# Kernel tuning notes

Hardware: AMD Instinct MI355X
Metric: run time of the kernel (lower is better)

Reference implementation:

```python
import jax, jax.numpy as jnp
import numpy as np

E, D, H, T = 8, 1024, 2048, 2048  # num_expert, d_model, d_hidden, tokens

def setup_inputs() -> dict:
    key = jax.random.key(0)
    ks = jax.random.split(key, 7)
    return {
        "moe_inp": jax.random.normal(ks[0], (T, D), jnp.float32),
        "Wg": jax.random.normal(ks[1], (D, E), jnp.float32) * 0.02,
        "bg": jnp.zeros((E,), jnp.float32),
        "W1": jax.random.normal(ks[2], (E, D, H), jnp.float32) * 0.02,
        "b1": jnp.zeros((E, H), jnp.float32),
        "W2": jax.random.normal(ks[3], (E, H, D), jnp.float32) * 0.02,
        "b2": jnp.zeros((E, D), jnp.float32),
        "top_k": 2,
    }

def reference(moe_inp, Wg, bg, W1, b1, W2, b2, top_k):
    # NaiveGate: linear gate, top-k select, softmax over the selected logits
    logits = moe_inp @ Wg + bg                      # [T, E]
    top_vals, top_idx = jax.lax.top_k(logits, top_k)  # [T, k]
    gate_score = jax.nn.softmax(top_vals, axis=-1)    # [T, k]

    # Exact (no capacity drop) MoE: scan over experts, mask-combine.
    # Equivalent math to scatter -> per-expert FFN -> gather -> bmm(gate_score, ...).
    def body(acc, xs):
        e, w1, bb1, w2, bb2 = xs
        h = jax.nn.gelu(moe_inp @ w1 + bb1)          # [T, H]
        y = h @ w2 + bb2                             # [T, D]
        w = jnp.sum(jnp.where(top_idx == e, gate_score, 0.0), axis=-1)  # [T]
        return acc + w[:, None] * y, None

    init = jnp.zeros_like(moe_inp)
    xs = (jnp.arange(E), W1, b1, W2, b2)
    moe_outp, _ = jax.lax.scan(body, init, xs)
    return moe_outp, top_idx
```

## Files before the change

### kernel.cpp

```cpp
#include <hip/hip_runtime.h>
#include <stdint.h>

#define T_TOK 2048
#define D_DIM 1024
#define H_DIM 2048
#define N_EXP 8
#define MAXS  4608

#define WS_CNT    0
#define WS_BTOK   256
#define WS_BW     (WS_BTOK + N_EXP*2048*4)
#define WS_XG     (WS_BW + N_EXP*2048*4)
#define WS_HBUF   (WS_XG + (size_t)MAXS*1024*2)
#define WS_W1T    (WS_HBUF + (size_t)MAXS*2048*2)
#define WS_W2T    (WS_W1T + (size_t)N_EXP*1024*2048*2)

typedef __bf16 bf16x8 __attribute__((ext_vector_type(8)));
typedef float  f32x4  __attribute__((ext_vector_type(4)));

__device__ __forceinline__ unsigned short f2bf(float f) {
  unsigned int u = __float_as_uint(f);
  u += 0x7fffu + ((u >> 16) & 1u);
  return (unsigned short)(u >> 16);
}

__device__ __forceinline__ float gelu_tanh(float x) {
  float u = 0.7978845608028654f * (x + 0.044715f * x * x * x);
  return 0.5f * x * (1.0f + tanhf(u));
}

__global__ void zero_kernel(float4* __restrict__ out4, int* __restrict__ cnt) {
  int i = blockIdx.x * 256 + threadIdx.x;
  out4[i] = make_float4(0.f, 0.f, 0.f, 0.f);
  if (blockIdx.x == 0 && threadIdx.x < N_EXP) cnt[threadIdx.x] = 0;
}

__global__ void gate_kernel(const float* __restrict__ x, const float* __restrict__ Wg,
                            const float* __restrict__ bg, float* __restrict__ out_idx,
                            int* __restrict__ cnt, int* __restrict__ btok,
                            float* __restrict__ bw) {
  const int lane = threadIdx.x & 63;
  const int t = blockIdx.x * 4 + (threadIdx.x >> 6);
  float p[8];
#pragma unroll
  for (int i = 0; i < 8; ++i) p[i] = 0.f;
  const float* xr = x + (size_t)t * D_DIM;
  for (int i = lane; i < D_DIM; i += 64) {
    const float xv = xr[i];
    const float4 wa = ((const float4*)(Wg + i * 8))[0];
    const float4 wb = ((const float4*)(Wg + i * 8))[1];
    p[0] += xv * wa.x; p[1] += xv * wa.y; p[2] += xv * wa.z; p[3] += xv * wa.w;
    p[4] += xv * wb.x; p[5] += xv * wb.y; p[6] += xv * wb.z; p[7] += xv * wb.w;
  }
#pragma unroll
  for (int off = 32; off > 0; off >>= 1) {
#pragma unroll
    for (int i = 0; i < 8; ++i) p[i] += __shfl_xor(p[i], off);
  }
  if (lane == 0) {
#pragma unroll
    for (int i = 0; i < 8; ++i) p[i] += bg[i];
    int i0 = 0; float v0 = p[0];
#pragma unroll
    for (int i = 1; i < 8; ++i) if (p[i] > v0) { v0 = p[i]; i0 = i; }
    int i1 = -1; float v1 = -3.4e38f;
#pragma unroll
    for (int i = 0; i < 8; ++i) if (i != i0 && p[i] > v1) { v1 = p[i]; i1 = i; }
    const float ex = expf(v1 - v0);
    const float inv = 1.f / (1.f + ex);
    out_idx[t * 2 + 0] = (float)i0;
    out_idx[t * 2 + 1] = (float)i1;
    int s0 = atomicAdd(&cnt[i0], 1);
    btok[i0 * 2048 + s0] = t; bw[i0 * 2048 + s0] = inv;
    int s1 = atomicAdd(&cnt[i1], 1);
    btok[i1 * 2048 + s1] = t; bw[i1 * 2048 + s1] = ex * inv;
  }
}

__global__ void transpose_cvt(const float* __restrict__ W1, unsigned short* __restrict__ W1t,
                              const float* __restrict__ W2, unsigned short* __restrict__ W2t) {
  const int set = blockIdx.z;
  const int e = blockIdx.y;
  const int lin = blockIdx.x;
  const int R = set ? H_DIM : D_DIM;
  const int C = set ? D_DIM : H_DIM;
  const int tx = set ? (lin & 15) : (lin & 31);
  const int ty = set ? (lin >> 4) : (lin >> 5);
  const float* in = (set ? W2 : W1) + (size_t)e * (D_DIM * H_DIM);
  unsigned short* out = (set ? W2t : W1t) + (size_t)e * (D_DIM * H_DIM);
  const int c0 = tx * 64, r0 = ty * 64;
  __shared__ float tile[64][68];
  const int tid = threadIdx.x;
#pragma unroll
  for (int p = 0; p < 4; ++p) {
    const int idx = p * 256 + tid;
    const int r = idx >> 4, c4 = idx & 15;
    *(float4*)&tile[r][c4 * 4] = *(const float4*)(in + (size_t)(r0 + r) * C + c0 + c4 * 4);
  }
  __syncthreads();
#pragma unroll
  for (int p = 0; p < 2; ++p) {
    const int idx = p * 256 + tid;
    const int oc = idx >> 3, seg = idx & 7;
    unsigned u[4];
#pragma unroll
    for (int j = 0; j < 4; ++j) {
      const unsigned lo = f2bf(tile[seg * 8 + 2 * j][oc]);
      const unsigned hi = f2bf(tile[seg * 8 + 2 * j + 1][oc]);
      u[j] = lo | (hi << 16);
    }
    *(uint4*)(out + (size_t)(c0 + oc) * R + r0 + seg * 8) = make_uint4(u[0], u[1], u[2], u[3]);
  }
}

__device__ __forceinline__ void expert_seg(const int* __restrict__ cnt, int e,
                                           int& base, int& ce, int& pcnt) {
  int off = 0; base = 0; ce = 0; pcnt = 0;
#pragma unroll
  for (int i = 0; i < N_EXP; ++i) {
    const int c = cnt[i];
    const int p = (c + 63) & ~63;
    if (i == e) { base = off; ce = c; pcnt = p; }
    off += p;
  }
}

__global__ void gather_cvt(const float* __restrict__ x, const int* __restrict__ cnt,
                           const int* __restrict__ btok, unsigned short* __restrict__ Xg) {
  const int s = blockIdx.x;
  int off = 0, e = -1, loc = 0, c_e = 0;
#pragma unroll
  for (int i = 0; i < N_EXP; ++i) {
    const int c = cnt[i];
    const int p = (c + 63) & ~63;
    if (e < 0 && s < off + p) { e = i; loc = s - off; c_e = c; }
    off += p;
  }
  if (e < 0) return;
  uint2* orow = (uint2*)(Xg + (size_t)s * D_DIM);
  if (loc < c_e) {
    const int t = btok[e * 2048 + loc];
    const float4 v = ((const float4*)(x + (size_t)t * D_DIM))[threadIdx.x];
    uint2 u;
    u.x = (unsigned)f2bf(v.x) | ((unsigned)f2bf(v.y) << 16);
    u.y = (unsigned)f2bf(v.z) | ((unsigned)f2bf(v.w) << 16);
    orow[threadIdx.x] = u;
  } else {
    orow[threadIdx.x] = make_uint2(0u, 0u);
  }
}

template <int MODE>
__global__ void __launch_bounds__(256, 3) moe_gemm(
    const unsigned short* __restrict__ A, const unsigned short* __restrict__ B,
    const float* __restrict__ bias, const int* __restrict__ cnt,
    const int* __restrict__ btok, const float* __restrict__ bw,
    unsigned short* __restrict__ Hout, float* __restrict__ out) {
  constexpr int K   = (MODE == 0) ? D_DIM : H_DIM;
  constexpr int SK  = (MODE == 0) ? 1 : 2;
  constexpr int KS  = K / SK;
  constexpr int NIT = KS / 64;

  const int lin = blockIdx.x;
  const int glo = lin & 7;
  const int mt  = (lin >> 3) & 31;
  const int g   = ((lin >> 8) << 3) | glo;
  int nt, e, ksl;
  if (MODE == 0) { nt = g & 15; e = g >> 4; ksl = 0; }
  else           { nt = g & 7;  e = (g >> 3) & 7; ksl = g >> 6; }

  int base, ce, pcnt;
  expert_seg(cnt, e, base, ce, pcnt);
  if (mt * 64 >= pcnt) return;
  const int row0 = base + mt * 64;
  const int n0 = nt * 128;

  __shared__ __align__(16) unsigned short As[2][64 * 64];
  __shared__ __align__(16) unsigned short Bs[2][128 * 64];

  const int tid = threadIdx.x;
  const int lane = tid & 63;
  const int wv = tid >> 6;
  const int wm = wv >> 1;
  const int wn = wv & 1;

  const unsigned short* Ab = A + (size_t)row0 * K + ksl * KS;
  const unsigned short* Bb = B + (size_t)e * ((size_t)H_DIM * D_DIM) + (size_t)n0 * K + ksl * KS;

  f32x4 acc[2][4];
#pragma unroll
  for (int i = 0; i < 2; ++i)
#pragma unroll
    for (int j = 0; j < 4; ++j) acc[i][j] = (f32x4)(0.0f);

  const int rloc = lane >> 3;
  const int q = lane & 7;
  const int gq = ((q - rloc) & 7) * 8;
  const int fr = lane & 15;
  const int kg = lane >> 4;

  auto stage = [&](int kt, int b) {
    const int k0 = kt * 64;
#pragma unroll
    for (int it = 0; it < 2; ++it) {
      const int ci = wv * 2 + it;
      const int r = ci * 8 + rloc;
      const unsigned short* ga = Ab + (size_t)r * K + (k0 + gq);
      __builtin_amdgcn_global_load_lds(
          (__attribute__((address_space(1))) void*)ga,
          (__attribute__((address_space(3))) void*)(As[b] + ci * 8 * 64), 16, 0, 0);
    }
#pragma unroll
    for (int it = 0; it < 4; ++it) {
      const int ci = wv * 4 + it;
      const int r = ci * 8 + rloc;
      const unsigned short* gb = Bb + (size_t)r * K + (k0 + gq);
      __builtin_amdgcn_global_load_lds(
          (__attribute__((address_space(1))) void*)gb,
          (__attribute__((address_space(3))) void*)(Bs[b] + ci * 8 * 64), 16, 0, 0);
    }
  };

  stage(0, 0);
  for (int i = 0; i < NIT; ++i) {
    const int b = i & 1;
    __syncthreads();
    if (i + 1 < NIT) stage(i + 1, b ^ 1);
    bf16x8 av[2][2], bv[2][4];
#pragma unroll
    for (int kk = 0; kk < 2; ++kk) {
#pragma unroll
      for (int mi = 0; mi < 2; ++mi) {
        const int rr = wm * 32 + mi * 16 + fr;
        const int slot = ((kk * 4 + kg) + (rr & 7)) & 7;
        av[kk][mi] = *(const bf16x8*)(As[b] + rr * 64 + slot * 8);
      }
#pragma unroll
      for (int ni = 0; ni < 4; ++ni) {
        const int rr = wn * 64 + ni * 16 + fr;
        const int slot = ((kk * 4 + kg) + (rr & 7)) & 7;
        bv[kk][ni] = *(const bf16x8*)(Bs[b] + rr * 64 + slot * 8);
      }
    }
#pragma unroll
    for (int kk = 0; kk < 2; ++kk)
#pragma unroll
      for (int mi = 0; mi < 2; ++mi)
#pragma unroll
        for (int ni = 0; ni < 4; ++ni)
          acc[mi][ni] = __builtin_amdgcn_mfma_f32_16x16x32_bf16(av[kk][mi], bv[kk][ni],
                                                                acc[mi][ni], 0, 0, 0);
  }

  if (MODE == 0) {
    const float* bb = bias + (size_t)e * H_DIM + n0;
#pragma unroll
    for (int mi = 0; mi < 2; ++mi) {
      const int rb = wm * 32 + mi * 16 + (lane >> 4) * 4;
#pragma unroll
      for (int r = 0; r < 4; ++r) {
        unsigned short* hp = Hout + (size_t)(row0 + rb + r) * H_DIM + n0;
#pragma unroll
        for (int ni = 0; ni < 4; ++ni) {
          const int col = wn * 64 + ni * 16 + fr;
          hp[col] = f2bf(gelu_tanh(acc[mi][ni][r] + bb[col]));
        }
      }
    }
  } else {
    const float* bb = bias + (size_t)e * D_DIM + n0;
#pragma unroll
    for (int mi = 0; mi < 2; ++mi) {
      const int rb = wm * 32 + mi * 16 + (lane >> 4) * 4;
#pragma unroll
      for (int r = 0; r < 4; ++r) {
        const int local = mt * 64 + rb + r;
        if (local < ce) {
          const int tok = btok[e * 2048 + local];
          const float w = bw[e * 2048 + local];
          float* op = out + (size_t)tok * D_DIM + n0;
#pragma unroll
          for (int ni = 0; ni < 4; ++ni) {
            const int col = wn * 64 + ni * 16 + fr;
            const float bias_once = (ksl == 0) ? bb[col] : 0.f;
            atomicAdd(op + col, w * (acc[mi][ni][r] + bias_once));
          }
        }
      }
    }
  }
}

extern "C" void kernel_launch(void* const* d_in, const int* in_sizes, int n_in,
                              void* d_out, int out_size, void* d_ws, size_t ws_size,
                              hipStream_t stream) {
  const float* moe_inp = (const float*)d_in[0];
  const float* Wg = (const float*)d_in[1];
  const float* bg = (const float*)d_in[2];
  const float* W1 = (const float*)d_in[3];
  const float* b1 = (const float*)d_in[4];
  const float* W2 = (const float*)d_in[5];
  const float* b2 = (const float*)d_in[6];
  float* out = (float*)d_out;

  char* ws = (char*)d_ws;
  int* cnt  = (int*)(ws + WS_CNT);
  int* btok = (int*)(ws + WS_BTOK);
  float* bw = (float*)(ws + WS_BW);
  unsigned short* Xg   = (unsigned short*)(ws + WS_XG);
  unsigned short* Hbuf = (unsigned short*)(ws + WS_HBUF);
  unsigned short* W1t  = (unsigned short*)(ws + WS_W1T);
  unsigned short* W2t  = (unsigned short*)(ws + WS_W2T);

  zero_kernel<<<dim3(2048), dim3(256), 0, stream>>>((float4*)out, cnt);
  gate_kernel<<<dim3(T_TOK / 4), dim3(256), 0, stream>>>(moe_inp, Wg, bg,
                                                         out + (size_t)T_TOK * D_DIM,
                                                         cnt, btok, bw);
  transpose_cvt<<<dim3(512, N_EXP, 2), dim3(256), 0, stream>>>(W1, W1t, W2, W2t);
  gather_cvt<<<dim3(MAXS), dim3(256), 0, stream>>>(moe_inp, cnt, btok, Xg);
  moe_gemm<0><<<dim3(4096), dim3(256), 0, stream>>>(
      Xg, W1t, b1, cnt, btok, bw, Hbuf, nullptr);
  moe_gemm<1><<<dim3(4096), dim3(256), 0, stream>>>(
      Hbuf, W2t, b2, cnt, btok, bw, nullptr, out);
}
```

Before: 345.7 us.

## Replace direct global-to-LDS loads with register-staged two-deep prefetch and XOR swizzle

The GEMM main loop swaps the global_load_lds direct copies for ordinary vector loads into registers, issued two k-tiles ahead. The registers are written into a double-buffered, XOR-swizzled LDS tile after the MFMAs, so global latency overlaps with compute. The transpose kernel also replaces its padded shared tile with an XOR-swizzled layout to avoid bank conflicts. This costs extra VGPRs for the staged tiles, which may lower occupancy, and adds LDS write instructions.

```diff
diff --git a/kernel.cpp b/kernel.cpp
--- a/kernel.cpp
+++ b/kernel.cpp
@@ -89,13 +89,14 @@
   const float* in = (set ? W2 : W1) + (size_t)e * (D_DIM * H_DIM);
   unsigned short* out = (set ? W2t : W1t) + (size_t)e * (D_DIM * H_DIM);
   const int c0 = tx * 64, r0 = ty * 64;
-  __shared__ float tile[64][68];
+  __shared__ float tile[64 * 64];
   const int tid = threadIdx.x;
 #pragma unroll
   for (int p = 0; p < 4; ++p) {
     const int idx = p * 256 + tid;
     const int r = idx >> 4, c4 = idx & 15;
-    *(float4*)&tile[r][c4 * 4] = *(const float4*)(in + (size_t)(r0 + r) * C + c0 + c4 * 4);
+    const float4 v = *(const float4*)(in + (size_t)(r0 + r) * C + c0 + c4 * 4);
+    *(float4*)&tile[(r * 16 + (c4 ^ (r & 15))) * 4] = v;
   }
   __syncthreads();
 #pragma unroll
@@ -105,9 +106,10 @@
     unsigned u[4];
 #pragma unroll
     for (int j = 0; j < 4; ++j) {
-      const unsigned lo = f2bf(tile[seg * 8 + 2 * j][oc]);
-      const unsigned hi = f2bf(tile[seg * 8 + 2 * j + 1][oc]);
-      u[j] = lo | (hi << 16);
+      const int ra = seg * 8 + 2 * j, rb = ra + 1;
+      const float fa = tile[(ra * 16 + ((oc >> 2) ^ (ra & 15))) * 4 + (oc & 3)];
+      const float fb = tile[(rb * 16 + ((oc >> 2) ^ (rb & 15))) * 4 + (oc & 3)];
+      u[j] = (unsigned)f2bf(fa) | ((unsigned)f2bf(fb) << 16);
     }
     *(uint4*)(out + (size_t)(c0 + oc) * R + r0 + seg * 8) = make_uint4(u[0], u[1], u[2], u[3]);
   }
@@ -184,64 +186,64 @@
   const int wm = wv >> 1;
   const int wn = wv & 1;
 
+  const int srow = tid >> 3;
+  const int sq = tid & 7;
+  const int lslot = (sq ^ (srow & 7)) * 8;
+
   const unsigned short* Ab = A + (size_t)row0 * K + ksl * KS;
   const unsigned short* Bb = B + (size_t)e * ((size_t)H_DIM * D_DIM) + (size_t)n0 * K + ksl * KS;
 
+  uint4 rA[2][2], rB[2][4];
+  auto loadS = [&](int kt, int s) {
+    const int k0 = kt * 64 + sq * 8;
+#pragma unroll
+    for (int c = 0; c < 2; ++c)
+      rA[s][c] = *(const uint4*)(Ab + (size_t)(srow + 32 * c) * K + k0);
+#pragma unroll
+    for (int c = 0; c < 4; ++c)
+      rB[s][c] = *(const uint4*)(Bb + (size_t)(srow + 32 * c) * K + k0);
+  };
+  auto writeS = [&](int s, int b) {
+#pragma unroll
+    for (int c = 0; c < 2; ++c)
+      *(uint4*)(As[b] + (srow + 32 * c) * 64 + lslot) = rA[s][c];
+#pragma unroll
+    for (int c = 0; c < 4; ++c)
+      *(uint4*)(Bs[b] + (srow + 32 * c) * 64 + lslot) = rB[s][c];
+  };
+
   f32x4 acc[2][4];
 #pragma unroll
   for (int i = 0; i < 2; ++i)
 #pragma unroll
     for (int j = 0; j < 4; ++j) acc[i][j] = (f32x4)(0.0f);
 
-  const int rloc = lane >> 3;
-  const int q = lane & 7;
-  const int gq = ((q - rloc) & 7) * 8;
   const int fr = lane & 15;
   const int kg = lane >> 4;
 
-  auto stage = [&](int kt, int b) {
-    const int k0 = kt * 64;
-#pragma unroll
-    for (int it = 0; it < 2; ++it) {
-      const int ci = wv * 2 + it;
-      const int r = ci * 8 + rloc;
-      const unsigned short* ga = Ab + (size_t)r * K + (k0 + gq);
-      __builtin_amdgcn_global_load_lds(
-          (__attribute__((address_space(1))) void*)ga,
-          (__attribute__((address_space(3))) void*)(As[b] + ci * 8 * 64), 16, 0, 0);
-    }
-#pragma unroll
-    for (int it = 0; it < 4; ++it) {
-      const int ci = wv * 4 + it;
-      const int r = ci * 8 + rloc;
-      const unsigned short* gb = Bb + (size_t)r * K + (k0 + gq);
-      __builtin_amdgcn_global_load_lds(
-          (__attribute__((address_space(1))) void*)gb,
-          (__attribute__((address_space(3))) void*)(Bs[b] + ci * 8 * 64), 16, 0, 0);
-    }
-  };
-
-  stage(0, 0);
+  loadS(0, 0);
+  loadS(1, 1);
+  writeS(0, 0);
+  __syncthreads();
+
   for (int i = 0; i < NIT; ++i) {
     const int b = i & 1;
-    __syncthreads();
-    if (i + 1 < NIT) stage(i + 1, b ^ 1);
     bf16x8 av[2][2], bv[2][4];
 #pragma unroll
     for (int kk = 0; kk < 2; ++kk) {
+      const int gA = kk * 4 + kg;
 #pragma unroll
       for (int mi = 0; mi < 2; ++mi) {
         const int rr = wm * 32 + mi * 16 + fr;
-        const int slot = ((kk * 4 + kg) + (rr & 7)) & 7;
-        av[kk][mi] = *(const bf16x8*)(As[b] + rr * 64 + slot * 8);
+        av[kk][mi] = *(const bf16x8*)(As[b] + rr * 64 + ((gA ^ (rr & 7)) * 8));
       }
 #pragma unroll
       for (int ni = 0; ni < 4; ++ni) {
         const int rr = wn * 64 + ni * 16 + fr;
-        const int slot = ((kk * 4 + kg) + (rr & 7)) & 7;
-        bv[kk][ni] = *(const bf16x8*)(Bs[b] + rr * 64 + slot * 8);
+        bv[kk][ni] = *(const bf16x8*)(Bs[b] + rr * 64 + ((gA ^ (rr & 7)) * 8));
       }
     }
+    if (i + 2 < NIT) loadS(i + 2, i & 1);
 #pragma unroll
     for (int kk = 0; kk < 2; ++kk)
 #pragma unroll
@@ -250,6 +252,8 @@
         for (int ni = 0; ni < 4; ++ni)
           acc[mi][ni] = __builtin_amdgcn_mfma_f32_16x16x32_bf16(av[kk][mi], bv[kk][ni],
                                                                 acc[mi][ni], 0, 0, 0);
+    if (i + 1 < NIT) writeS((i + 1) & 1, b ^ 1);
+    __syncthreads();
   }
 
   if (MODE == 0) {
```

Measured after the change: 560.5 us. 1.62x slower.

## Retile expert GEMMs to 256x256 blocks with 512 threads and swizzle transpose LDS

Applied to the files above, without the earlier changes.

Both expert GEMMs move from 64x128 tiles with 256 threads and K-step 64 to 256x256 tiles with 512 threads (8 waves), K-step 32, and a 128-element accumulator per thread. This raises data reuse per LDS load and cuts the grid from 4096 to 512 launched blocks. The weight transpose kernel also swaps its padded shared tile for an XOR-swizzled layout to avoid bank conflicts. The risks are that far fewer blocks fill the CUs when each expert holds only about 512 rows, and that register pressure rises sharply. Rows that overrun an expert's padded segment are now masked on write.

```diff
diff --git a/kernel.cpp b/kernel.cpp
--- a/kernel.cpp
+++ b/kernel.cpp
@@ -89,13 +89,14 @@
   const float* in = (set ? W2 : W1) + (size_t)e * (D_DIM * H_DIM);
   unsigned short* out = (set ? W2t : W1t) + (size_t)e * (D_DIM * H_DIM);
   const int c0 = tx * 64, r0 = ty * 64;
-  __shared__ float tile[64][68];
+  __shared__ float tile[64 * 64];
   const int tid = threadIdx.x;
 #pragma unroll
   for (int p = 0; p < 4; ++p) {
     const int idx = p * 256 + tid;
     const int r = idx >> 4, c4 = idx & 15;
-    *(float4*)&tile[r][c4 * 4] = *(const float4*)(in + (size_t)(r0 + r) * C + c0 + c4 * 4);
+    const float4 v = *(const float4*)(in + (size_t)(r0 + r) * C + c0 + c4 * 4);
+    *(float4*)&tile[(r * 16 + (c4 ^ (r & 15))) * 4] = v;
   }
   __syncthreads();
 #pragma unroll
@@ -105,9 +106,10 @@
     unsigned u[4];
 #pragma unroll
     for (int j = 0; j < 4; ++j) {
-      const unsigned lo = f2bf(tile[seg * 8 + 2 * j][oc]);
-      const unsigned hi = f2bf(tile[seg * 8 + 2 * j + 1][oc]);
-      u[j] = lo | (hi << 16);
+      const int ra = seg * 8 + 2 * j, rb = ra + 1;
+      const float fa = tile[(ra * 16 + ((oc >> 2) ^ (ra & 15))) * 4 + (oc & 3)];
+      const float fb = tile[(rb * 16 + ((oc >> 2) ^ (rb & 15))) * 4 + (oc & 3)];
+      u[j] = (unsigned)f2bf(fa) | ((unsigned)f2bf(fb) << 16);
     }
     *(uint4*)(out + (size_t)(c0 + oc) * R + r0 + seg * 8) = make_uint4(u[0], u[1], u[2], u[3]);
   }
@@ -151,7 +153,7 @@
 }
 
 template <int MODE>
-__global__ void __launch_bounds__(256, 3) moe_gemm(
+__global__ void __launch_bounds__(512, 2) moe_gemm(
     const unsigned short* __restrict__ A, const unsigned short* __restrict__ B,
     const float* __restrict__ bias, const int* __restrict__ cnt,
     const int* __restrict__ btok, const float* __restrict__ bw,
@@ -159,122 +161,115 @@
   constexpr int K   = (MODE == 0) ? D_DIM : H_DIM;
   constexpr int SK  = (MODE == 0) ? 1 : 2;
   constexpr int KS  = K / SK;
-  constexpr int NIT = KS / 64;
+  constexpr int NIT = KS / 32;
+  constexpr int NT  = ((MODE == 0) ? H_DIM : D_DIM) / 256;
 
   const int lin = blockIdx.x;
-  const int glo = lin & 7;
-  const int mt  = (lin >> 3) & 31;
-  const int g   = ((lin >> 8) << 3) | glo;
-  int nt, e, ksl;
-  if (MODE == 0) { nt = g & 15; e = g >> 4; ksl = 0; }
-  else           { nt = g & 7;  e = (g >> 3) & 7; ksl = g >> 6; }
+  int nt, e, ksl, mt;
+  if (MODE == 0) { nt = lin & 7; e = (lin >> 3) & 7; ksl = 0; mt = lin >> 6; }
+  else           { nt = lin & 3; e = (lin >> 2) & 7; ksl = (lin >> 5) & 1; mt = lin >> 6; }
+  (void)NT;
 
   int base, ce, pcnt;
   expert_seg(cnt, e, base, ce, pcnt);
-  if (mt * 64 >= pcnt) return;
-  const int row0 = base + mt * 64;
-  const int n0 = nt * 128;
-
-  __shared__ __align__(16) unsigned short As[2][64 * 64];
-  __shared__ __align__(16) unsigned short Bs[2][128 * 64];
+  if (mt * 256 >= pcnt) return;
+  const int row0 = base + mt * 256;
+  const int n0 = nt * 256;
+
+  __shared__ __align__(16) unsigned short As[2][256 * 32];
+  __shared__ __align__(16) unsigned short Bs[2][256 * 32];
 
   const int tid = threadIdx.x;
   const int lane = tid & 63;
   const int wv = tid >> 6;
-  const int wm = wv >> 1;
-  const int wn = wv & 1;
+  const int wm = wv >> 2;
+  const int wn = wv & 3;
 
   const unsigned short* Ab = A + (size_t)row0 * K + ksl * KS;
   const unsigned short* Bb = B + (size_t)e * ((size_t)H_DIM * D_DIM) + (size_t)n0 * K + ksl * KS;
 
-  f32x4 acc[2][4];
-#pragma unroll
-  for (int i = 0; i < 2; ++i)
+  const int rloc = lane >> 2;
+  const int q = lane & 3;
+  const int gq = ((q - (rloc >> 1)) & 3) * 8;
+
+  auto stage = [&](int kt, int b) {
+    const int k0 = kt * 32;
+#pragma unroll
+    for (int it = 0; it < 2; ++it) {
+      const int ci = wv * 2 + it;
+      const int r = ci * 16 + rloc;
+      __builtin_amdgcn_global_load_lds(
+          (__attribute__((address_space(1))) void*)(Ab + (size_t)r * K + (k0 + gq)),
+          (__attribute__((address_space(3))) void*)(As[b] + ci * 512), 16, 0, 0);
+    }
+#pragma unroll
+    for (int it = 0; it < 2; ++it) {
+      const int ci = wv * 2 + it;
+      const int r = ci * 16 + rloc;
+      __builtin_amdgcn_global_load_lds(
+          (__attribute__((address_space(1))) void*)(Bb + (size_t)r * K + (k0 + gq)),
+          (__attribute__((address_space(3))) void*)(Bs[b] + ci * 512), 16, 0, 0);
+    }
+  };
+
+  f32x4 acc[8][4];
+#pragma unroll
+  for (int i = 0; i < 8; ++i)
 #pragma unroll
     for (int j = 0; j < 4; ++j) acc[i][j] = (f32x4)(0.0f);
 
-  const int rloc = lane >> 3;
-  const int q = lane & 7;
-  const int gq = ((q - rloc) & 7) * 8;
   const int fr = lane & 15;
   const int kg = lane >> 4;
-
-  auto stage = [&](int kt, int b) {
-    const int k0 = kt * 64;
-#pragma unroll
-    for (int it = 0; it < 2; ++it) {
-      const int ci = wv * 2 + it;
-      const int r = ci * 8 + rloc;
-      const unsigned short* ga = Ab + (size_t)r * K + (k0 + gq);
-      __builtin_amdgcn_global_load_lds(
-          (__attribute__((address_space(1))) void*)ga,
-          (__attribute__((address_space(3))) void*)(As[b] + ci * 8 * 64), 16, 0, 0);
-    }
-#pragma unroll
-    for (int it = 0; it < 4; ++it) {
-      const int ci = wv * 4 + it;
-      const int r = ci * 8 + rloc;
-      const unsigned short* gb = Bb + (size_t)r * K + (k0 + gq);
-      __builtin_amdgcn_global_load_lds(
-          (__attribute__((address_space(1))) void*)gb,
-          (__attribute__((address_space(3))) void*)(Bs[b] + ci * 8 * 64), 16, 0, 0);
-    }
-  };
 
   stage(0, 0);
   for (int i = 0; i < NIT; ++i) {
     const int b = i & 1;
     __syncthreads();
     if (i + 1 < NIT) stage(i + 1, b ^ 1);
-    bf16x8 av[2][2], bv[2][4];
-#pragma unroll
-    for (int kk = 0; kk < 2; ++kk) {
-#pragma unroll
-      for (int mi = 0; mi < 2; ++mi) {
-        const int rr = wm * 32 + mi * 16 + fr;
-        const int slot = ((kk * 4 + kg) + (rr & 7)) & 7;
-        av[kk][mi] = *(const bf16x8*)(As[b] + rr * 64 + slot * 8);
-      }
-#pragma unroll
-      for (int ni = 0; ni < 4; ++ni) {
-        const int rr = wn * 64 + ni * 16 + fr;
-        const int slot = ((kk * 4 + kg) + (rr & 7)) & 7;
-        bv[kk][ni] = *(const bf16x8*)(Bs[b] + rr * 64 + slot * 8);
-      }
-    }
-#pragma unroll
-    for (int kk = 0; kk < 2; ++kk)
-#pragma unroll
-      for (int mi = 0; mi < 2; ++mi)
-#pragma unroll
-        for (int ni = 0; ni < 4; ++ni)
-          acc[mi][ni] = __builtin_amdgcn_mfma_f32_16x16x32_bf16(av[kk][mi], bv[kk][ni],
-                                                                acc[mi][ni], 0, 0, 0);
+    bf16x8 av[8], bv[4];
+#pragma unroll
+    for (int mi = 0; mi < 8; ++mi) {
+      const int rr = wm * 128 + mi * 16 + fr;
+      av[mi] = *(const bf16x8*)(As[b] + rr * 32 + (((kg + (rr >> 1)) & 3) * 8));
+    }
+#pragma unroll
+    for (int ni = 0; ni < 4; ++ni) {
+      const int rr = wn * 64 + ni * 16 + fr;
+      bv[ni] = *(const bf16x8*)(Bs[b] + rr * 32 + (((kg + (rr >> 1)) & 3) * 8));
+    }
+#pragma unroll
+    for (int mi = 0; mi < 8; ++mi)
+#pragma unroll
+      for (int ni = 0; ni < 4; ++ni)
+        acc[mi][ni] = __builtin_amdgcn_mfma_f32_16x16x32_bf16(av[mi], bv[ni], acc[mi][ni], 0, 0, 0);
   }
 
   if (MODE == 0) {
     const float* bb = bias + (size_t)e * H_DIM + n0;
 #pragma unroll
-    for (int mi = 0; mi < 2; ++mi) {
-      const int rb = wm * 32 + mi * 16 + (lane >> 4) * 4;
+    for (int mi = 0; mi < 8; ++mi) {
+      const int rb = wm * 128 + mi * 16 + kg * 4;
 #pragma unroll
       for (int r = 0; r < 4; ++r) {
-        unsigned short* hp = Hout + (size_t)(row0 + rb + r) * H_DIM + n0;
-#pragma unroll
-        for (int ni = 0; ni < 4; ++ni) {
-          const int col = wn * 64 + ni * 16 + fr;
-          hp[col] = f2bf(gelu_tanh(acc[mi][ni][r] + bb[col]));
+        const int local = mt * 256 + rb + r;
+        if (local < pcnt) {
+          unsigned short* hp = Hout + (size_t)(row0 + rb + r) * H_DIM + n0;
+#pragma unroll
+          for (int ni = 0; ni < 4; ++ni) {
+            const int col = wn * 64 + ni * 16 + fr;
+            hp[col] = f2bf(gelu_tanh(acc[mi][ni][r] + bb[col]));
+          }
         }
       }
     }
   } else {
     const float* bb = bias + (size_t)e * D_DIM + n0;
 #pragma unroll
-    for (int mi = 0; mi < 2; ++mi) {
-      const int rb = wm * 32 + mi * 16 + (lane >> 4) * 4;
+    for (int mi = 0; mi < 8; ++mi) {
+      const int rb = wm * 128 + mi * 16 + kg * 4;
 #pragma unroll
       for (int r = 0; r < 4; ++r) {
-        const int local = mt * 64 + rb + r;
+        const int local = mt * 256 + rb + r;
         if (local < ce) {
           const int tok = btok[e * 2048 + local];
           const float w = bw[e * 2048 + local];
@@ -318,8 +313,8 @@
                                                          cnt, btok, bw);
   transpose_cvt<<<dim3(512, N_EXP, 2), dim3(256), 0, stream>>>(W1, W1t, W2, W2t);
   gather_cvt<<<dim3(MAXS), dim3(256), 0, stream>>>(moe_inp, cnt, btok, Xg);
-  moe_gemm<0><<<dim3(4096), dim3(256), 0, stream>>>(
+  moe_gemm<0><<<dim3(512), dim3(512), 0, stream>>>(
       Xg, W1t, b1, cnt, btok, bw, Hbuf, nullptr);
-  moe_gemm<1><<<dim3(4096), dim3(256), 0, stream>>>(
+  moe_gemm<1><<<dim3(512), dim3(512), 0, stream>>>(
       Hbuf, W2t, b2, cnt, btok, bw, nullptr, out);
 }
```

After: 399.9 us. 1.16x slower.
